# Kernel tuning notes

Measured on AMD Instinct MI355X. Metric: run time of the kernel, lower is better.

## Reference

```python
import jax, jax.numpy as jnp
import numpy as np


def _soft_proto(x, P):
    d2 = (x * x).sum(-1, keepdims=True) - 2.0 * (x @ P.T) + (P * P).sum(-1)
    w = jax.nn.softmax(-d2, axis=-1)  # scores = -dist_sq, softmax over K
    return w @ P  # soft-matched prototypes


def setup_inputs() -> dict:
    key = jax.random.key(0)
    ks = jax.random.split(key, 12)
    B = 1024
    def u(k, shape, s=0.1):
        return jax.random.uniform(k, shape, minval=-s, maxval=s, dtype=jnp.float32)
    return {
        "fcn": jax.random.normal(ks[0], (B, 90, 90), jnp.float32),
        "scn": jax.random.normal(ks[1], (B, 90, 90), jnp.float32),
        # node embedding Linear(90->48), weights stored [in,out]
        "W_node": u(ks[2], (90, 48)), "b_node": jnp.zeros((48,), jnp.float32),
        "P_node": u(ks[3], (64, 48)),   # node prototypes, init uniform(-0.1,0.1)
        "W_graph": u(ks[4], (48, 32)), "b_graph": jnp.zeros((32,), jnp.float32),
        "P_graph": u(ks[5], (32, 32)),
        "Wg1": u(ks[6], (32, 32)), "bg1": jnp.zeros((32,), jnp.float32),
        "Wg2": u(ks[7], (32, 16)), "bg2": jnp.zeros((16,), jnp.float32),
        "P_cls": u(ks[8], (16, 16)),
        # classifier: final_dim = 2*90*48 + 2*32 + 2*16 = 8736
        "Wc1": u(ks[9], (8736, 256)), "bc1": jnp.zeros((256,), jnp.float32),
        "Wc2": u(ks[10], (256, 3)), "bc2": jnp.zeros((3,), jnp.float32),
    }


def reference(fcn, scn, W_node, b_node, P_node, W_graph, b_graph, P_graph,
              Wg1, bg1, Wg2, bg2, P_cls, Wc1, bc1, Wc2, bc2):
    def branch(x):
        nodes = x @ W_node + b_node                  # [B,90,48]
        nm = _soft_proto(nodes, P_node)              # [B,90,48]
        eg = nm.mean(axis=1) @ W_graph + b_graph     # [B,32]
        gp = _soft_proto(eg, P_graph)                # [B,32]
        ec = jax.nn.relu(gp @ Wg1 + bg1) @ Wg2 + bg2 # [B,16]
        cp = _soft_proto(ec, P_cls)                  # [B,16]
        return nm, gp, cp

    nmf, gpf, cpf = branch(fcn)
    nms, gps, cps = branch(scn)
    B = fcn.shape[0]
    R = jnp.concatenate(
        [nmf.reshape(B, -1), nms.reshape(B, -1), gpf, gps, cpf, cps], axis=-1)  # [B,8736]
    # dropout(0.5) is identity in eval mode
    logits = jax.nn.relu(R @ Wc1 + bc1) @ Wc2 + bc2  # [B,3]
    return logits
```

## Files before the change

kernel.cpp:

```cpp
#include <hip/hip_runtime.h>
#include <hip/hip_bf16.h>

using f16   = _Float16;
using f16x4 = __attribute__((ext_vector_type(4))) _Float16;
using f16x8 = __attribute__((ext_vector_type(8))) _Float16;
using f32x4 = __attribute__((ext_vector_type(4))) float;

__global__ __launch_bounds__(256) void prep_kernel(
    const float* __restrict__ Wn, const float* __restrict__ Pn,
    f16* __restrict__ wf, float* __restrict__ q)
{
  int i = blockIdx.x * 256 + threadIdx.x;
  if (i < 4992) {
    int n = i / 104, k = i - n * 104;
    wf[i] = (k < 90) ? (f16)Wn[k * 48 + n] : (f16)0.f;
  } else if (i < 8576) {
    int j = i - 4992; int p = j / 56, c = j - p * 56;
    wf[i] = (c < 48) ? (f16)Pn[p * 48 + c] : (f16)0.f;
  } else if (i < 12032) {
    int j = i - 8576; int r = j / 72, p = j - r * 72;
    wf[i] = (p < 64) ? (f16)Pn[p * 48 + r] : (f16)0.f;
  } else if (i < 12096) {
    int p = i - 12032;
    float s = 0.f;
    for (int j = 0; j < 48; ++j) { float v = Pn[p * 48 + j]; s = fmaf(v, v, s); }
    q[p] = s;
  }
}

__global__ __launch_bounds__(256) void wc1t_kernel(
    const float* __restrict__ Wc1, f16* __restrict__ Wc1T)
{
  __shared__ f16 sT[32 * 36];
  const int tid = threadIdx.x;
  const int kt = blockIdx.x, ct = blockIdx.y;
  const int c = tid & 31, r4 = (tid >> 5) * 4;
  #pragma unroll
  for (int i = 0; i < 4; ++i) {
    int r = r4 + i;
    sT[c * 36 + r] = (f16)Wc1[(size_t)(kt * 32 + r) * 256 + ct * 32 + c];
  }
  __syncthreads();
  #pragma unroll
  for (int i = 0; i < 4; ++i) {
    int r = r4 + i;
    Wc1T[(size_t)(ct * 32 + r) * 8736 + kt * 32 + c] = sT[r * 36 + c];
  }
}

__global__ __launch_bounds__(256, 4) void node_kernel(
    const float* __restrict__ fcn, const float* __restrict__ scn,
    const float* __restrict__ bn, const f16* __restrict__ wf,
    const float* __restrict__ qg,
    f16* __restrict__ R, float* __restrict__ nmmean)
{
  __shared__ __align__(16) f16 uR[96 * 104];
  __shared__ __align__(16) f16 sNodes[96 * 56];
  __shared__ float sQ[64];
  __shared__ float sMean[96];

  f16* sX = uR;
  f16* sW = uR;
  const f16* Pw   = wf + 4992;
  const f16* PnTw = wf + 8576;

  const int tid = threadIdx.x;
  const int lane = tid & 63, wv = tid >> 6;
  const int l15 = lane & 15, lg = lane >> 4;
  const int b = blockIdx.x, br = blockIdx.y;

  const float* x = (br ? scn : fcn) + (size_t)b * 8100;
  for (int u = tid; u < 1152; u += 256) {
    const int r = u / 12, c = u - r * 12;
    f16x8 h;
    #pragma unroll
    for (int e = 0; e < 8; ++e) h[e] = (f16)0.f;
    if (r < 90) {
      const float* src = x + r * 90 + c * 8;
      if (c < 11) {
        float2 a0 = *(const float2*)(src + 0);
        float2 a1 = *(const float2*)(src + 2);
        float2 a2 = *(const float2*)(src + 4);
        float2 a3 = *(const float2*)(src + 6);
        h[0] = (f16)a0.x; h[1] = (f16)a0.y; h[2] = (f16)a1.x; h[3] = (f16)a1.y;
        h[4] = (f16)a2.x; h[5] = (f16)a2.y; h[6] = (f16)a3.x; h[7] = (f16)a3.y;
      } else {
        float2 a0 = *(const float2*)src;
        h[0] = (f16)a0.x; h[1] = (f16)a0.y;
      }
    }
    *(f16x8*)&sX[r * 104 + c * 8] = h;
  }
  if (tid < 64) sQ[tid] = qg[tid];
  __syncthreads();

  for (int t = wv; t < 18; t += 4) {
    const int mt = t / 3, nt = t - 3 * mt;
    f32x4 acc = {0.f, 0.f, 0.f, 0.f};
    #pragma unroll
    for (int kt = 0; kt < 3; ++kt) {
      f16x8 a  = *(const f16x8*)&sX[(mt * 16 + l15) * 104 + kt * 32 + lg * 8];
      f16x8 bb = *(const f16x8*)&wf[(nt * 16 + l15) * 104 + kt * 32 + lg * 8];
      acc = __builtin_amdgcn_mfma_f32_16x16x32_f16(a, bb, acc, 0, 0, 0);
    }
    const float bias = bn[nt * 16 + l15];
    #pragma unroll
    for (int r = 0; r < 4; ++r)
      sNodes[(mt * 16 + lg * 4 + r) * 56 + nt * 16 + l15] = (f16)(acc[r] + bias);
  }
  __syncthreads();

  for (int mt = wv; mt < 6; mt += 4) {
    f32x4 acc[4];
    #pragma unroll
    for (int nt = 0; nt < 4; ++nt) acc[nt] = (f32x4){0.f, 0.f, 0.f, 0.f};
    const f16x8 a0 = *(const f16x8*)&sNodes[(mt * 16 + l15) * 56 + lg * 8];
    const f16x4 a1 = *(const f16x4*)&sNodes[(mt * 16 + l15) * 56 + 32 + lg * 4];
    #pragma unroll
    for (int nt = 0; nt < 4; ++nt) {
      f16x8 b0 = *(const f16x8*)&Pw[(nt * 16 + l15) * 56 + lg * 8];
      acc[nt] = __builtin_amdgcn_mfma_f32_16x16x32_f16(a0, b0, acc[nt], 0, 0, 0);
      f16x4 b1 = *(const f16x4*)&Pw[(nt * 16 + l15) * 56 + 32 + lg * 4];
      acc[nt] = __builtin_amdgcn_mfma_f32_16x16x16f16(a1, b1, acc[nt], 0, 0, 0);
    }
    float qv[4];
    #pragma unroll
    for (int nt = 0; nt < 4; ++nt) qv[nt] = sQ[nt * 16 + l15];
    #pragma unroll
    for (int r = 0; r < 4; ++r) {
      float s0 = 2.f * acc[0][r] - qv[0];
      float s1 = 2.f * acc[1][r] - qv[1];
      float s2 = 2.f * acc[2][r] - qv[2];
      float s3 = 2.f * acc[3][r] - qv[3];
      float m = fmaxf(fmaxf(s0, s1), fmaxf(s2, s3));
      m = fmaxf(m, __shfl_xor(m, 1, 64));
      m = fmaxf(m, __shfl_xor(m, 2, 64));
      m = fmaxf(m, __shfl_xor(m, 4, 64));
      m = fmaxf(m, __shfl_xor(m, 8, 64));
      float e0 = __expf(s0 - m), e1 = __expf(s1 - m);
      float e2 = __expf(s2 - m), e3 = __expf(s3 - m);
      float sum = (e0 + e1) + (e2 + e3);
      sum += __shfl_xor(sum, 1, 64);
      sum += __shfl_xor(sum, 2, 64);
      sum += __shfl_xor(sum, 4, 64);
      sum += __shfl_xor(sum, 8, 64);
      const float inv = 1.f / sum;
      const int row = mt * 16 + lg * 4 + r;
      sW[row * 72 + 0 * 16 + l15] = (f16)(e0 * inv);
      sW[row * 72 + 1 * 16 + l15] = (f16)(e1 * inv);
      sW[row * 72 + 2 * 16 + l15] = (f16)(e2 * inv);
      sW[row * 72 + 3 * 16 + l15] = (f16)(e3 * inv);
    }
  }
  __syncthreads();

  f16* Rrow = R + (size_t)b * 8736 + (size_t)br * 4320;
  for (int t = wv; t < 18; t += 4) {
    const int mt = t / 3, nt = t - 3 * mt;
    f32x4 acc = {0.f, 0.f, 0.f, 0.f};
    #pragma unroll
    for (int kt = 0; kt < 2; ++kt) {
      f16x8 a  = *(const f16x8*)&sW[(mt * 16 + l15) * 72 + kt * 32 + lg * 8];
      f16x8 bb = *(const f16x8*)&PnTw[(nt * 16 + l15) * 72 + kt * 32 + lg * 8];
      acc = __builtin_amdgcn_mfma_f32_16x16x32_f16(a, bb, acc, 0, 0, 0);
    }
    #pragma unroll
    for (int r = 0; r < 4; ++r) {
      const int row = mt * 16 + lg * 4 + r;
      const f16 hv = (f16)acc[r];
      sNodes[row * 56 + nt * 16 + l15] = hv;
      if (row < 90) Rrow[row * 48 + nt * 16 + l15] = hv;
    }
  }
  __syncthreads();

  if (tid < 96) {
    int j = tid < 48 ? tid : tid - 48;
    int h = tid < 48 ? 0 : 1;
    float s = 0.f;
    for (int i = h * 45; i < h * 45 + 45; ++i) s += (float)sNodes[i * 56 + j];
    sMean[tid] = s;
  }
  __syncthreads();
  if (tid < 48) {
    nmmean[((size_t)br * 1024 + b) * 48 + tid] =
        (sMean[tid] + sMean[48 + tid]) * (1.f / 90.f);
  }
}

__global__ __launch_bounds__(256) void graph_kernel(
    const float* __restrict__ nmmean,
    const float* __restrict__ Wg, const float* __restrict__ bg,
    const float* __restrict__ Pg,
    const float* __restrict__ Wg1, const float* __restrict__ bg1,
    const float* __restrict__ Wg2, const float* __restrict__ bg2,
    const float* __restrict__ Pc,
    f16* __restrict__ R)
{
  __shared__ float sE[4][64];
  __shared__ float sT[4][64];
  const int tid = threadIdx.x;
  const int wid = tid >> 6, lane = tid & 63;
  const int idx = blockIdx.x * 4 + wid;
  const int br = idx >> 10, b = idx & 1023;
  const float* mrow = nmmean + (size_t)idx * 48;
  f16* Rrow = R + (size_t)b * 8736;

  if (lane < 32) {
    float e = bg[lane];
    #pragma unroll
    for (int k = 0; k < 48; ++k) e = fmaf(mrow[k], Wg[k * 32 + lane], e);
    sE[wid][lane] = e;
  }
  __syncthreads();
  if (lane < 32) {
    float s = 0.f;
    #pragma unroll
    for (int j = 0; j < 32; ++j) { float pv = Pg[lane * 32 + j]; s += pv * (2.f * sE[wid][j] - pv); }
    float m = s;
    for (int d = 16; d >= 1; d >>= 1) m = fmaxf(m, __shfl_xor(m, d, 64));
    float ex = __expf(s - m);
    float sum = ex;
    for (int d = 16; d >= 1; d >>= 1) sum += __shfl_xor(sum, d, 64);
    sT[wid][lane] = ex / sum;
  }
  __syncthreads();
  if (lane < 32) {
    float g = 0.f;
    #pragma unroll
    for (int p = 0; p < 32; ++p) g = fmaf(sT[wid][p], Pg[p * 32 + lane], g);
    Rrow[8640 + br * 32 + lane] = (f16)g;
    sE[wid][lane] = g;
  }
  __syncthreads();
  if (lane < 32) {
    float h = bg1[lane];
    #pragma unroll
    for (int k = 0; k < 32; ++k) h = fmaf(sE[wid][k], Wg1[k * 32 + lane], h);
    sT[wid][lane] = fmaxf(h, 0.f);
  }
  __syncthreads();
  if (lane < 16) {
    float c = bg2[lane];
    #pragma unroll
    for (int k = 0; k < 32; ++k) c = fmaf(sT[wid][k], Wg2[k * 16 + lane], c);
    sE[wid][lane] = c;
  }
  __syncthreads();
  if (lane < 16) {
    float s = 0.f;
    #pragma unroll
    for (int j = 0; j < 16; ++j) { float pv = Pc[lane * 16 + j]; s += pv * (2.f * sE[wid][j] - pv); }
    float m = s;
    for (int d = 8; d >= 1; d >>= 1) m = fmaxf(m, __shfl_xor(m, d, 64));
    float ex = __expf(s - m);
    float sum = ex;
    for (int d = 8; d >= 1; d >>= 1) sum += __shfl_xor(sum, d, 64);
    sT[wid][lane] = ex / sum;
  }
  __syncthreads();
  if (lane < 16) {
    float c = 0.f;
    #pragma unroll
    for (int p = 0; p < 16; ++p) c = fmaf(sT[wid][p], Pc[p * 16 + lane], c);
    Rrow[8704 + br * 16 + lane] = (f16)c;
  }
}

__global__ __launch_bounds__(256) void gemm1_kernel(
    const f16* __restrict__ R, const f16* __restrict__ Wc1T,
    float* __restrict__ part, int KS)
{
  __shared__ __align__(16) f16 sA[128 * 40];
  __shared__ __align__(16) f16 sB[64 * 40];
  const int tid = threadIdx.x;
  const int lane = tid & 63, wv = tid >> 6;
  const int l15 = lane & 15, lg = lane >> 4;
  const int wm = wv >> 1, wn = wv & 1;
  const int bm = blockIdx.x * 128, bnc = blockIdx.y * 64, z = blockIdx.z;
  const int base = 273 / KS, rem = 273 - base * KS;
  const int t0 = z * base + (z < rem ? z : rem);
  const int nt_ = base + (z < rem ? 1 : 0);
  const int kbeg = t0 * 32, kend = (t0 + nt_) * 32;

  const int ar = tid >> 1, ah = (tid & 1) * 16;
  const int bc = tid >> 2, bh = (tid & 3) * 8;

  f32x4 acc[4][2];
  #pragma unroll
  for (int mt = 0; mt < 4; ++mt)
    #pragma unroll
    for (int nt = 0; nt < 2; ++nt) acc[mt][nt] = (f32x4){0.f, 0.f, 0.f, 0.f};

  for (int kk = kbeg; kk < kend; kk += 32) {
    const f16* asrc = &R[(size_t)(bm + ar) * 8736 + kk + ah];
    f16x8 v0 = *(const f16x8*)asrc;
    f16x8 v1 = *(const f16x8*)(asrc + 8);
    f16x8 w0 = *(const f16x8*)&Wc1T[(size_t)(bnc + bc) * 8736 + kk + bh];
    *(f16x8*)&sA[ar * 40 + ah] = v0;
    *(f16x8*)&sA[ar * 40 + ah + 8] = v1;
    *(f16x8*)&sB[bc * 40 + bh] = w0;
    __syncthreads();
    #pragma unroll
    for (int mt = 0; mt < 4; ++mt) {
      f16x8 a = *(const f16x8*)&sA[(wm * 64 + mt * 16 + l15) * 40 + lg * 8];
      #pragma unroll
      for (int nt = 0; nt < 2; ++nt) {
        f16x8 bb = *(const f16x8*)&sB[(wn * 32 + nt * 16 + l15) * 40 + lg * 8];
        acc[mt][nt] = __builtin_amdgcn_mfma_f32_16x16x32_f16(a, bb, acc[mt][nt], 0, 0, 0);
      }
    }
    __syncthreads();
  }
  float* pz = part + (size_t)z * 262144;
  #pragma unroll
  for (int mt = 0; mt < 4; ++mt)
    #pragma unroll
    for (int nt = 0; nt < 2; ++nt)
      #pragma unroll
      for (int r = 0; r < 4; ++r)
        pz[(size_t)(bm + wm * 64 + mt * 16 + lg * 4 + r) * 256 +
           bnc + wn * 32 + nt * 16 + l15] = acc[mt][nt][r];
}

__global__ __launch_bounds__(256) void head_kernel(
    const float* __restrict__ part, const float* __restrict__ bc1,
    const float* __restrict__ Wc2, const float* __restrict__ bc2,
    float* __restrict__ out, int KS)
{
  __shared__ float red[3][4];
  const int b = blockIdx.x, t = threadIdx.x;
  float acc = bc1[t];
  for (int z = 0; z < KS; ++z) acc += part[(size_t)z * 262144 + (size_t)b * 256 + t];
  float h = fmaxf(acc, 0.f);
  float p0 = h * Wc2[t * 3 + 0];
  float p1 = h * Wc2[t * 3 + 1];
  float p2 = h * Wc2[t * 3 + 2];
  for (int d = 32; d >= 1; d >>= 1) {
    p0 += __shfl_xor(p0, d, 64);
    p1 += __shfl_xor(p1, d, 64);
    p2 += __shfl_xor(p2, d, 64);
  }
  const int wid = t >> 6, lane = t & 63;
  if (lane == 0) { red[0][wid] = p0; red[1][wid] = p1; red[2][wid] = p2; }
  __syncthreads();
  if (t < 3) {
    out[(size_t)b * 3 + t] = red[t][0] + red[t][1] + red[t][2] + red[t][3] + bc2[t];
  }
}

extern "C" void kernel_launch(void* const* d_in, const int* in_sizes, int n_in,
                              void* d_out, int out_size, void* d_ws, size_t ws_size,
                              hipStream_t stream) {
  const float* fcn     = (const float*)d_in[0];
  const float* scn     = (const float*)d_in[1];
  const float* W_node  = (const float*)d_in[2];
  const float* b_node  = (const float*)d_in[3];
  const float* P_node  = (const float*)d_in[4];
  const float* W_graph = (const float*)d_in[5];
  const float* b_graph = (const float*)d_in[6];
  const float* P_graph = (const float*)d_in[7];
  const float* Wg1     = (const float*)d_in[8];
  const float* bg1     = (const float*)d_in[9];
  const float* Wg2     = (const float*)d_in[10];
  const float* bg2     = (const float*)d_in[11];
  const float* P_cls   = (const float*)d_in[12];
  const float* Wc1     = (const float*)d_in[13];
  const float* bc1     = (const float*)d_in[14];
  const float* Wc2     = (const float*)d_in[15];
  const float* bc2     = (const float*)d_in[16];
  float* out = (float*)d_out;

  char* ws = (char*)d_ws;
  f16*   R16    = (f16*)ws;
  f16*   Wc1T   = (f16*)(ws + 17891328);
  f16*   wf     = (f16*)(ws + 22364160);
  float* qbuf   = (float*)(ws + 22388224);
  float* nmmean = (float*)(ws + 22388480);
  float* part   = (float*)(ws + 22781696);

  size_t avail = ws_size > 22781696u ? ws_size - 22781696u : 0;
  int KS = (int)(avail / 1048576u);
  if (KS > 16) KS = 16;
  if (KS < 1) KS = 1;

  prep_kernel<<<48, 256, 0, stream>>>(W_node, P_node, wf, qbuf);
  wc1t_kernel<<<dim3(273, 8), 256, 0, stream>>>(Wc1, Wc1T);
  node_kernel<<<dim3(1024, 2), 256, 0, stream>>>(fcn, scn, b_node, wf, qbuf,
                                                 R16, nmmean);
  graph_kernel<<<512, 256, 0, stream>>>(nmmean, W_graph, b_graph, P_graph,
                                        Wg1, bg1, Wg2, bg2, P_cls, R16);
  gemm1_kernel<<<dim3(8, 4, KS), 256, 0, stream>>>(R16, Wc1T, part, KS);
  head_kernel<<<1024, 256, 0, stream>>>(part, bc1, Wc2, bc2, out, KS);
}
```

Before: 76.16 us.

## Load node-kernel input straight into MFMA registers, bypassing shared staging

The input tile is no longer staged in shared memory before the first node-embedding MFMA. Each wave now loads its 16-row slice of x from global memory directly into A-fragment registers and reuses it across all three output tiles. This removes a shared-memory round trip and one barrier, and it shrinks the shared buffer so launch bounds can rise from 4 to 6 blocks per CU. The cost is uncoalesced strided global loads per lane and possible register pressure under the tighter launch bound.

```diff
diff --git a/kernel.cpp b/kernel.cpp
--- a/kernel.cpp
+++ b/kernel.cpp
@@ -48,19 +48,17 @@
   }
 }
 
-__global__ __launch_bounds__(256, 4) void node_kernel(
+__global__ __launch_bounds__(256, 6) void node_kernel(
     const float* __restrict__ fcn, const float* __restrict__ scn,
     const float* __restrict__ bn, const f16* __restrict__ wf,
     const float* __restrict__ qg,
     f16* __restrict__ R, float* __restrict__ nmmean)
 {
-  __shared__ __align__(16) f16 uR[96 * 104];
+  __shared__ __align__(16) f16 sW[96 * 72];
   __shared__ __align__(16) f16 sNodes[96 * 56];
   __shared__ float sQ[64];
   __shared__ float sMean[96];
 
-  f16* sX = uR;
-  f16* sW = uR;
   const f16* Pw   = wf + 4992;
   const f16* PnTw = wf + 8576;
 
@@ -68,45 +66,49 @@
   const int lane = tid & 63, wv = tid >> 6;
   const int l15 = lane & 15, lg = lane >> 4;
   const int b = blockIdx.x, br = blockIdx.y;
-
   const float* x = (br ? scn : fcn) + (size_t)b * 8100;
-  for (int u = tid; u < 1152; u += 256) {
-    const int r = u / 12, c = u - r * 12;
-    f16x8 h;
-    #pragma unroll
-    for (int e = 0; e < 8; ++e) h[e] = (f16)0.f;
-    if (r < 90) {
-      const float* src = x + r * 90 + c * 8;
-      if (c < 11) {
-        float2 a0 = *(const float2*)(src + 0);
-        float2 a1 = *(const float2*)(src + 2);
-        float2 a2 = *(const float2*)(src + 4);
-        float2 a3 = *(const float2*)(src + 6);
-        h[0] = (f16)a0.x; h[1] = (f16)a0.y; h[2] = (f16)a1.x; h[3] = (f16)a1.y;
-        h[4] = (f16)a2.x; h[5] = (f16)a2.y; h[6] = (f16)a3.x; h[7] = (f16)a3.y;
-      } else {
-        float2 a0 = *(const float2*)src;
-        h[0] = (f16)a0.x; h[1] = (f16)a0.y;
+
+  if (tid < 64) sQ[tid] = qg[tid];
+
+  for (int mt = wv; mt < 6; mt += 4) {
+    const int row = mt * 16 + l15;
+    const float* xrow = x + row * 90;
+    f16x8 a[3];
+    #pragma unroll
+    for (int kt = 0; kt < 3; ++kt) {
+      const int k0 = kt * 32 + lg * 8;
+      f16x8 h;
+      #pragma unroll
+      for (int e = 0; e < 8; ++e) h[e] = (f16)0.f;
+      if (row < 90) {
+        const float* src = xrow + k0;
+        if (k0 < 88) {
+          float2 u0 = *(const float2*)(src + 0);
+          float2 u1 = *(const float2*)(src + 2);
+          float2 u2 = *(const float2*)(src + 4);
+          float2 u3 = *(const float2*)(src + 6);
+          h[0] = (f16)u0.x; h[1] = (f16)u0.y; h[2] = (f16)u1.x; h[3] = (f16)u1.y;
+          h[4] = (f16)u2.x; h[5] = (f16)u2.y; h[6] = (f16)u3.x; h[7] = (f16)u3.y;
+        } else {
+          float2 u0 = *(const float2*)src;
+          h[0] = (f16)u0.x; h[1] = (f16)u0.y;
+        }
       }
-    }
-    *(f16x8*)&sX[r * 104 + c * 8] = h;
-  }
-  if (tid < 64) sQ[tid] = qg[tid];
-  __syncthreads();
-
-  for (int t = wv; t < 18; t += 4) {
-    const int mt = t / 3, nt = t - 3 * mt;
-    f32x4 acc = {0.f, 0.f, 0.f, 0.f};
-    #pragma unroll
-    for (int kt = 0; kt < 3; ++kt) {
-      f16x8 a  = *(const f16x8*)&sX[(mt * 16 + l15) * 104 + kt * 32 + lg * 8];
-      f16x8 bb = *(const f16x8*)&wf[(nt * 16 + l15) * 104 + kt * 32 + lg * 8];
-      acc = __builtin_amdgcn_mfma_f32_16x16x32_f16(a, bb, acc, 0, 0, 0);
-    }
-    const float bias = bn[nt * 16 + l15];
-    #pragma unroll
-    for (int r = 0; r < 4; ++r)
-      sNodes[(mt * 16 + lg * 4 + r) * 56 + nt * 16 + l15] = (f16)(acc[r] + bias);
+      a[kt] = h;
+    }
+    #pragma unroll
+    for (int nt = 0; nt < 3; ++nt) {
+      f32x4 acc = {0.f, 0.f, 0.f, 0.f};
+      #pragma unroll
+      for (int kt = 0; kt < 3; ++kt) {
+        f16x8 bb = *(const f16x8*)&wf[(nt * 16 + l15) * 104 + kt * 32 + lg * 8];
+        acc = __builtin_amdgcn_mfma_f32_16x16x32_f16(a[kt], bb, acc, 0, 0, 0);
+      }
+      const float bias = bn[nt * 16 + l15];
+      #pragma unroll
+      for (int r = 0; r < 4; ++r)
+        sNodes[(mt * 16 + lg * 4 + r) * 56 + nt * 16 + l15] = (f16)(acc[r] + bias);
+    }
   }
   __syncthreads();
 
```

Result: no change. 74.93 us (-1.6%).
